# Performance work log

Hardware: AMD Instinct MI355X
Metric: run time of the kernel (lower is better)

The kernel has to match this reference:

```python
import jax, jax.numpy as jnp
import numpy as np

B, S, V, H, NH, DFF, L, T = 16, 256, 30522, 768, 12, 3072, 12, 9
DH = H // NH
LN_EPS = 1e-12


def _ln(x, g, b):
    m = x.mean(-1, keepdims=True)
    v = ((x - m) ** 2).mean(-1, keepdims=True)
    return (x - m) * jax.lax.rsqrt(v + LN_EPS) * g + b


def setup_inputs() -> dict:
    key = jax.random.key(0)
    ks = jax.random.split(key, 20)
    n = lambda k, shp: jax.random.normal(k, shp, jnp.float32) * 0.02
    return {
        "x": jax.random.randint(ks[0], (B, S), 0, V),
        "target": jax.random.randint(ks[1], (B, S), 0, T),
        "word_emb": n(ks[2], (V, H)),
        "pos_emb": n(ks[3], (S, H)),
        "type_emb": n(ks[4], (2, H)),
        "emb_ln_g": jnp.ones((H,)), "emb_ln_b": jnp.zeros((H,)),
        "Wq": n(ks[5], (L, H, H)), "bq": jnp.zeros((L, H)),
        "Wk": n(ks[6], (L, H, H)), "bk": jnp.zeros((L, H)),
        "Wv": n(ks[7], (L, H, H)), "bv": jnp.zeros((L, H)),
        "Wo": n(ks[8], (L, H, H)), "bo": jnp.zeros((L, H)),
        "ln1_g": jnp.ones((L, H)), "ln1_b": jnp.zeros((L, H)),
        "W1": n(ks[9], (L, H, DFF)), "b1": jnp.zeros((L, DFF)),
        "W2": n(ks[10], (L, DFF, H)), "b2": jnp.zeros((L, H)),
        "ln2_g": jnp.ones((L, H)), "ln2_b": jnp.zeros((L, H)),
        "clf_W": n(ks[11], (H, T)), "clf_b": jnp.zeros((T,)),
        "crf_start": jax.random.uniform(ks[12], (T,), jnp.float32, -0.1, 0.1),
        "crf_trans": jax.random.uniform(ks[13], (T, T), jnp.float32, -0.1, 0.1),
        "crf_end": jax.random.uniform(ks[14], (T,), jnp.float32, -0.1, 0.1),
    }


def _forward(x, target, word_emb, pos_emb, type_emb, emb_ln_g, emb_ln_b,
             Wq, bq, Wk, bk, Wv, bv, Wo, bo, ln1_g, ln1_b,
             W1, b1, W2, b2, ln2_g, ln2_b, clf_W, clf_b,
             crf_start, crf_trans, crf_end):
    # ---- BERT-base encoder (post-LN), no attention mask (all tokens valid) ----
    h = _ln(word_emb[x] + pos_emb[None, :, :] + type_emb[0][None, None, :], emb_ln_g, emb_ln_b)
    scale = 1.0 / np.sqrt(DH).astype(np.float32)
    for l in range(L):
        q = (h @ Wq[l] + bq[l]).reshape(B, S, NH, DH)
        k = (h @ Wk[l] + bk[l]).reshape(B, S, NH, DH)
        v = (h @ Wv[l] + bv[l]).reshape(B, S, NH, DH)
        att = jax.nn.softmax(jnp.einsum('bqhd,bkhd->bhqk', q, k) * scale, axis=-1)
        ctx = jnp.einsum('bhqk,bkhd->bqhd', att, v).reshape(B, S, H)
        h = _ln(h + ctx @ Wo[l] + bo[l], ln1_g[l], ln1_b[l])
        ff = jax.nn.gelu(h @ W1[l] + b1[l], approximate=False) @ W2[l] + b2[l]
        h = _ln(h + ff, ln2_g[l], ln2_b[l])

    logits = h @ clf_W + clf_b  # [B,S,T] emissions

    # ---- CRF negative log-likelihood (torchcrf semantics, reduction='mean') ----
    mask = target > -1                      # [B,S] bool
    tags = jnp.where(mask, target, 0)
    bidx = jnp.arange(B)
    emit = jnp.take_along_axis(logits, tags[..., None], axis=-1)[..., 0]  # [B,S]

    # numerator: score of the gold path
    num = crf_start[tags[:, 0]] + emit[:, 0]
    trans = crf_trans[tags[:, :-1], tags[:, 1:]]                          # [B,S-1]
    num = num + jnp.sum((trans + emit[:, 1:]) * mask[:, 1:], axis=1)
    last = jnp.sum(mask.astype(jnp.int32), axis=1) - 1
    num = num + crf_end[tags[bidx, last]]

    # denominator: forward algorithm (logsumexp recurrence over time)
    alpha0 = crf_start[None, :] + logits[:, 0]                            # [B,T]

    def step(alpha, xs):
        em, m = xs                                                        # [B,T], [B]
        nxt = jax.nn.logsumexp(alpha[:, :, None] + crf_trans[None], axis=1) + em
        return jnp.where(m[:, None], nxt, alpha), None

    alpha, _ = jax.lax.scan(step, alpha0,
                            (jnp.swapaxes(logits[:, 1:], 0, 1),
                             jnp.swapaxes(mask[:, 1:], 0, 1)))
    denom = jax.nn.logsumexp(alpha + crf_end[None, :], axis=1)

    llh = num - denom
    return -jnp.mean(llh)  # model returns -loss where loss = mean log-likelihood


def reference(x, target, word_emb, pos_emb, type_emb, emb_ln_g, emb_ln_b,
              Wq, bq, Wk, bk, Wv, bv, Wo, bo, ln1_g, ln1_b,
              W1, b1, W2, b2, ln2_g, ln2_b, clf_W, clf_b,
              crf_start, crf_trans, crf_end):
    return _forward(x, target, word_emb, pos_emb, type_emb, emb_ln_g, emb_ln_b,
                    Wq, bq, Wk, bk, Wv, bv, Wo, bo, ln1_g, ln1_b,
                    W1, b1, W2, b2, ln2_g, ln2_b, clf_W, clf_b,
                    crf_start, crf_trans, crf_end)
```

## Files before the change

### kernel.cpp

```cpp
#include <hip/hip_runtime.h>
#include <math.h>

#define B 16
#define S 256
#define H 768
#define NH 12
#define DH 64
#define DFF 3072
#define L 12
#define T 9
#define M (B*S)
#define LN_EPS 1e-12f
#define QKVS (3*H)
#define NCH 16

typedef __attribute__((ext_vector_type(8))) __bf16 bf16x8;
typedef __attribute__((ext_vector_type(8))) unsigned short u16x8;
typedef __attribute__((ext_vector_type(4))) unsigned short u16x4;
typedef __attribute__((ext_vector_type(4))) float f32x4;

__device__ __forceinline__ unsigned short f2bf(float f) {
    unsigned int u = __float_as_uint(f);
    unsigned int r = u + 0x7fffu + ((u >> 16) & 1u);
    return (unsigned short)(r >> 16);
}
__device__ __forceinline__ float bf2f(unsigned short h) {
    return __uint_as_float((unsigned int)h << 16);
}

__global__ void convT_kernel(const float* __restrict__ W, unsigned short* __restrict__ WT,
                             int K, int N, size_t dstLayerStride) {
    __shared__ float tile[32][33];
    const int layer = blockIdx.z;
    const float* Wp = W + (size_t)layer * K * N;
    unsigned short* Tp = WT + (size_t)layer * dstLayerStride;
    const int n0 = blockIdx.x * 32, k0 = blockIdx.y * 32;
    const int tx = threadIdx.x, ty = threadIdx.y;
#pragma unroll
    for (int i = 0; i < 32; i += 8)
        tile[ty + i][tx] = Wp[(size_t)(k0 + ty + i) * N + n0 + tx];
    __syncthreads();
    {
        const int u = ty * 32 + tx;
        const int r = u >> 3, kq = (u & 7) << 2;
        u16x4 o;
#pragma unroll
        for (int j = 0; j < 4; ++j) o[j] = f2bf(tile[kq + j][r]);
        *(u16x4*)&Tp[(size_t)(n0 + r) * K + k0 + kq] = o;
    }
}

__global__ void biascat_kernel(const float* __restrict__ bq, const float* __restrict__ bk,
                               const float* __restrict__ bv, float* __restrict__ out) {
    int idx = blockIdx.x * 256 + threadIdx.x;
    if (idx >= L * QKVS) return;
    int l = idx / QKVS, c = idx % QKVS;
    float v = (c < H) ? bq[l * H + c] : (c < 2 * H) ? bk[l * H + c - H] : bv[l * H + c - 2 * H];
    out[idx] = v;
}

__global__ void embed_ln_kernel(const int* __restrict__ x,
                                const float* __restrict__ word_emb,
                                const float* __restrict__ pos_emb,
                                const float* __restrict__ type_emb,
                                const float* __restrict__ g,
                                const float* __restrict__ bta,
                                float* __restrict__ h,
                                unsigned short* __restrict__ hb) {
    const int row = blockIdx.x;
    const int s = row % S;
    const int tok = x[row];
    const int t = threadIdx.x;
    const int c = t << 2;
    const float4 wv = *(const float4*)&word_emb[(size_t)tok * H + c];
    const float4 pv = *(const float4*)&pos_emb[s * H + c];
    const float4 tv = *(const float4*)&type_emb[c];
    float v[4] = {wv.x + pv.x + tv.x, wv.y + pv.y + tv.y, wv.z + pv.z + tv.z, wv.w + pv.w + tv.w};
    float s1 = v[0] + v[1] + v[2] + v[3];
    float s2 = v[0]*v[0] + v[1]*v[1] + v[2]*v[2] + v[3]*v[3];
#pragma unroll
    for (int o = 32; o; o >>= 1) { s1 += __shfl_xor(s1, o); s2 += __shfl_xor(s2, o); }
    __shared__ float ws[3][2];
    const int w = t >> 6, l = t & 63;
    if (l == 0) { ws[w][0] = s1; ws[w][1] = s2; }
    __syncthreads();
    const float S1 = ws[0][0] + ws[1][0] + ws[2][0];
    const float S2 = ws[0][1] + ws[1][1] + ws[2][1];
    const float mean = S1 * (1.0f / H);
    const float var = fmaxf(S2 * (1.0f / H) - mean * mean, 0.f);
    const float inv = rsqrtf(var + LN_EPS);
    const float4 gv = *(const float4*)&g[c];
    const float4 bv = *(const float4*)&bta[c];
    float4 outv;
    outv.x = (v[0] - mean) * inv * gv.x + bv.x;
    outv.y = (v[1] - mean) * inv * gv.y + bv.y;
    outv.z = (v[2] - mean) * inv * gv.z + bv.z;
    outv.w = (v[3] - mean) * inv * gv.w + bv.w;
    *(float4*)&h[(size_t)row * H + c] = outv;
    u16x4 ob = {f2bf(outv.x), f2bf(outv.y), f2bf(outv.z), f2bf(outv.w)};
    *(u16x4*)&hb[(size_t)row * H + c] = ob;
}

__global__ void residual_ln_kernel(float* __restrict__ h,
                                   const unsigned short* __restrict__ delta,
                                   const float* __restrict__ g,
                                   const float* __restrict__ bta,
                                   unsigned short* __restrict__ hb) {
    const int row = blockIdx.x;
    const int t = threadIdx.x;
    const int c = t << 2;
    const float4 hv = *(const float4*)&h[(size_t)row * H + c];
    const u16x4 dv4 = *(const u16x4*)&delta[(size_t)row * H + c];
    float v[4] = {hv.x + bf2f(dv4[0]), hv.y + bf2f(dv4[1]), hv.z + bf2f(dv4[2]), hv.w + bf2f(dv4[3])};
    float s1 = v[0] + v[1] + v[2] + v[3];
    float s2 = v[0]*v[0] + v[1]*v[1] + v[2]*v[2] + v[3]*v[3];
#pragma unroll
    for (int o = 32; o; o >>= 1) { s1 += __shfl_xor(s1, o); s2 += __shfl_xor(s2, o); }
    __shared__ float ws[3][2];
    const int w = t >> 6, l = t & 63;
    if (l == 0) { ws[w][0] = s1; ws[w][1] = s2; }
    __syncthreads();
    const float S1 = ws[0][0] + ws[1][0] + ws[2][0];
    const float S2 = ws[0][1] + ws[1][1] + ws[2][1];
    const float mean = S1 * (1.0f / H);
    const float var = fmaxf(S2 * (1.0f / H) - mean * mean, 0.f);
    const float inv = rsqrtf(var + LN_EPS);
    const float4 gv = *(const float4*)&g[c];
    const float4 bv = *(const float4*)&bta[c];
    float4 outv;
    outv.x = (v[0] - mean) * inv * gv.x + bv.x;
    outv.y = (v[1] - mean) * inv * gv.y + bv.y;
    outv.z = (v[2] - mean) * inv * gv.z + bv.z;
    outv.w = (v[3] - mean) * inv * gv.w + bv.w;
    *(float4*)&h[(size_t)row * H + c] = outv;
    u16x4 ob = {f2bf(outv.x), f2bf(outv.y), f2bf(outv.z), f2bf(outv.w)};
    *(u16x4*)&hb[(size_t)row * H + c] = ob;
}

#define LSTR 72

template<int ACT, int WF, int WB, int MR>
__global__ __launch_bounds__(256, 3)
void gemm_bf16(const unsigned short* __restrict__ A,
               const unsigned short* __restrict__ WT,
               const float* __restrict__ bias,
               float* __restrict__ Cf,
               unsigned short* __restrict__ Cb,
               int K, int N) {
    __shared__ unsigned short lA[MR * 32 * LSTR];
    __shared__ unsigned short lB[128 * LSTR];
    const int tid = threadIdx.x;
    const int m0 = blockIdx.y * (MR * 32), n0 = blockIdx.x << 7;
    const int l = tid & 63, w = tid >> 6;
    const int wr = w >> 1, wc = w & 1;
    const int lr = l & 15, kg = l >> 4;

    const int srow = tid >> 3, scol = (tid & 7) << 3;
    const unsigned short* gA = A + (size_t)(m0 + srow) * K + scol;
    const unsigned short* gB = WT + (size_t)(n0 + srow) * K + scol;

    f32x4 acc[MR][4];
#pragma unroll
    for (int i = 0; i < MR; ++i)
#pragma unroll
        for (int j = 0; j < 4; ++j) acc[i][j] = (f32x4){0.f, 0.f, 0.f, 0.f};

    u16x8 ra[MR], rb[4];
#pragma unroll
    for (int p = 0; p < MR; ++p) ra[p] = *(const u16x8*)(gA + (size_t)p * 32 * K);
#pragma unroll
    for (int p = 0; p < 4; ++p) rb[p] = *(const u16x8*)(gB + (size_t)p * 32 * K);

    for (int kt = 0; kt < K; kt += 64) {
#pragma unroll
        for (int p = 0; p < MR; ++p)
            *(u16x8*)&lA[(srow + p * 32) * LSTR + scol] = ra[p];
#pragma unroll
        for (int p = 0; p < 4; ++p)
            *(u16x8*)&lB[(srow + p * 32) * LSTR + scol] = rb[p];
        __syncthreads();
        if (kt + 64 < K) {
#pragma unroll
            for (int p = 0; p < MR; ++p) ra[p] = *(const u16x8*)(gA + (size_t)p * 32 * K + kt + 64);
#pragma unroll
            for (int p = 0; p < 4; ++p) rb[p] = *(const u16x8*)(gB + (size_t)p * 32 * K + kt + 64);
        }
#pragma unroll
        for (int ks = 0; ks < 2; ++ks) {
            bf16x8 af[MR], bfr[4];
#pragma unroll
            for (int m = 0; m < MR; ++m)
                af[m] = *(const bf16x8*)&lA[(wr * (MR * 16) + (m << 4) + lr) * LSTR + ks * 32 + (kg << 3)];
#pragma unroll
            for (int n = 0; n < 4; ++n)
                bfr[n] = *(const bf16x8*)&lB[((wc << 6) + (n << 4) + lr) * LSTR + ks * 32 + (kg << 3)];
#pragma unroll
            for (int m = 0; m < MR; ++m)
#pragma unroll
                for (int n = 0; n < 4; ++n)
                    acc[m][n] = __builtin_amdgcn_mfma_f32_16x16x32_bf16(af[m], bfr[n], acc[m][n], 0, 0, 0);
        }
        __syncthreads();
    }

    const int rbase = m0 + wr * (MR * 16) + (kg << 2);
    const int cbase = n0 + (wc << 6) + lr;
#pragma unroll
    for (int m = 0; m < MR; ++m) {
#pragma unroll
        for (int n = 0; n < 4; ++n) {
            const int col = cbase + (n << 4);
            const float bv = bias[col];
#pragma unroll
            for (int j = 0; j < 4; ++j) {
                const int row = rbase + (m << 4) + j;
                float v = acc[m][n][j] + bv;
                if (ACT == 1) v = 0.5f * v * (1.0f + erff(v * 0.70710678118654752440f));
                if (WF) Cf[(size_t)row * N + col] = v;
                if (WB) Cb[(size_t)row * N + col] = f2bf(v);
            }
        }
    }
}

__global__ __launch_bounds__(256, 2)
void attn_mfma(const unsigned short* __restrict__ qkv,
               unsigned short* __restrict__ ctxb) {
    __shared__ unsigned short Ks[256 * 72];
    __shared__ unsigned short Vt[64 * 264];
    __shared__ unsigned short Ps[4][16 * 72];

    const int blk = blockIdx.x;
    const int half = blk & 1;
    const int hh = (blk >> 1) % NH;
    const int b = blk / (2 * NH);
    const int t = threadIdx.x;
    const int l = t & 63, w = t >> 6;
    const int l15 = l & 15, g = l >> 4;

    {
        const int c0 = (t & 7) << 3;
        int r = t >> 3;
#pragma unroll
        for (int it = 0; it < 8; ++it, r += 32) {
            u16x8 kv = *(const u16x8*)&qkv[(size_t)(b * S + r) * QKVS + H + hh * 64 + c0];
            *(u16x8*)&Ks[r * 72 + c0] = kv;
        }
    }
    {
        const int d0 = (t & 7) << 3;
        int s = t >> 3;
#pragma unroll
        for (int it = 0; it < 8; ++it, s += 32) {
            u16x8 vv = *(const u16x8*)&qkv[(size_t)(b * S + s) * QKVS + 2 * H + hh * 64 + d0];
#pragma unroll
            for (int j = 0; j < 8; ++j) {
                int d = d0 + j;
                Vt[d * 264 + (s ^ (((d >> 3) & 7) << 3))] = vv[j];
            }
        }
    }
    __syncthreads();

    unsigned short* ps = Ps[w];
#pragma unroll
    for (int qi = 0; qi < 2; ++qi) {
        const int qrow = half * 128 + qi * 64 + w * 16 + l15;
        const unsigned short* qp = &qkv[(size_t)(b * S + qrow) * QKVS + hh * 64 + g * 8];
        bf16x8 aq0 = *(const bf16x8*)qp;
        bf16x8 aq1 = *(const bf16x8*)(qp + 32);

        f32x4 acc[16];
#pragma unroll
        for (int n = 0; n < 16; ++n) acc[n] = (f32x4){0.f, 0.f, 0.f, 0.f};
        __builtin_amdgcn_s_setprio(1);
#pragma unroll
        for (int n = 0; n < 16; ++n) {
            const unsigned short* kp = &Ks[(n * 16 + l15) * 72 + g * 8];
            bf16x8 b0 = *(const bf16x8*)kp;
            bf16x8 b1 = *(const bf16x8*)(kp + 32);
            acc[n] = __builtin_amdgcn_mfma_f32_16x16x32_bf16(aq0, b0, acc[n], 0, 0, 0);
            acc[n] = __builtin_amdgcn_mfma_f32_16x16x32_bf16(aq1, b1, acc[n], 0, 0, 0);
        }
        __builtin_amdgcn_s_setprio(0);

        float inv[4];
#pragma unroll
        for (int j = 0; j < 4; ++j) {
            float mx = acc[0][j];
#pragma unroll
            for (int n = 1; n < 16; ++n) mx = fmaxf(mx, acc[n][j]);
            mx = fmaxf(mx, __shfl_xor(mx, 1));
            mx = fmaxf(mx, __shfl_xor(mx, 2));
            mx = fmaxf(mx, __shfl_xor(mx, 4));
            mx = fmaxf(mx, __shfl_xor(mx, 8));
            float sum = 0.f;
#pragma unroll
            for (int n = 0; n < 16; ++n) {
                float e = exp2f((acc[n][j] - mx) * 0.18033688011112042f);
                acc[n][j] = e;
                sum += e;
            }
            sum += __shfl_xor(sum, 1);
            sum += __shfl_xor(sum, 2);
            sum += __shfl_xor(sum, 4);
            sum += __shfl_xor(sum, 8);
            inv[j] = 1.0f / sum;
        }

        f32x4 cacc[4];
#pragma unroll
        for (int nd = 0; nd < 4; ++nd) cacc[nd] = (f32x4){0.f, 0.f, 0.f, 0.f};
#pragma unroll
        for (int c = 0; c < 4; ++c) {
#pragma unroll
            for (int nl = 0; nl < 4; ++nl) {
                int n = c * 4 + nl;
#pragma unroll
                for (int j = 0; j < 4; ++j)
                    ps[(g * 4 + j) * 72 + nl * 16 + l15] = f2bf(acc[n][j]);
            }
            bf16x8 pa0 = *(const bf16x8*)&ps[l15 * 72 + g * 8];
            bf16x8 pa1 = *(const bf16x8*)&ps[l15 * 72 + 32 + g * 8];
            __builtin_amdgcn_s_setprio(1);
#pragma unroll
            for (int nd = 0; nd < 4; ++nd) {
                const int d = nd * 16 + l15;
                const int swz = ((d >> 3) & 7) << 3;
                const unsigned short* vp0 = &Vt[d * 264 + ((c * 64 + g * 8) ^ swz)];
                const unsigned short* vp1 = &Vt[d * 264 + ((c * 64 + 32 + g * 8) ^ swz)];
                bf16x8 v0 = *(const bf16x8*)vp0;
                bf16x8 v1 = *(const bf16x8*)vp1;
                cacc[nd] = __builtin_amdgcn_mfma_f32_16x16x32_bf16(pa0, v0, cacc[nd], 0, 0, 0);
                cacc[nd] = __builtin_amdgcn_mfma_f32_16x16x32_bf16(pa1, v1, cacc[nd], 0, 0, 0);
            }
            __builtin_amdgcn_s_setprio(0);
        }

#pragma unroll
        for (int nd = 0; nd < 4; ++nd)
#pragma unroll
            for (int j = 0; j < 4; ++j) {
                int qr = half * 128 + qi * 64 + w * 16 + g * 4 + j;
                ctxb[(size_t)(b * S + qr) * H + hh * 64 + nd * 16 + l15] = f2bf(cacc[nd][j] * inv[j]);
            }
    }
}

__global__ void clf_kernel(const float* __restrict__ h,
                           const float* __restrict__ W,
                           const float* __restrict__ bias,
                           float* __restrict__ logits) {
    const int row = blockIdx.x * 4 + (threadIdx.x >> 6);
    const int l = threadIdx.x & 63;
    const float* hp = h + (size_t)row * H;
    float acc[T] = {};
#pragma unroll
    for (int i = 0; i < 12; ++i) {
        const int k = l + (i << 6);
        const float x = hp[k];
        const float* wp = &W[k * T];
#pragma unroll
        for (int n = 0; n < T; ++n) acc[n] += x * wp[n];
    }
#pragma unroll
    for (int o = 32; o; o >>= 1)
#pragma unroll
        for (int n = 0; n < T; ++n) acc[n] += __shfl_xor(acc[n], o);
    if (l < T) logits[(size_t)row * T + l] = acc[l] + bias[l];
}

__global__ void crf_chunk_kernel(const float* __restrict__ logits,
                                 const int* __restrict__ target,
                                 const float* __restrict__ trans,
                                 float* __restrict__ Tc) {
    const int blk = blockIdx.x;
    const int b = blk >> 4, c = blk & 15;
    const int t = threadIdx.x;
    const int i = t / 9, j = t - i * 9;
    const bool act = t < 81;
    __shared__ float Tb[2][81];
    const float* lg = logits + (size_t)b * S * T;
    const int* tg = target + b * S;
    const float K2 = 1.44269504088896340736f;
    const float IK = 0.69314718055994530942f;

    float trc[T];
    if (act) {
#pragma unroll
        for (int k = 0; k < T; ++k) trc[k] = trans[k * T + j];
        Tb[0][t] = (i == j) ? 0.f : -1e30f;
    }
    __syncthreads();

    int p = 0;
    const int s0 = c * 16 + 1;
    const int s1 = (c == 15) ? S : (s0 + 16);
    for (int s = s0; s < s1; ++s) {
        if (tg[s] > -1) {
            if (act) {
                const float em = lg[s * T + j];
                float v[T];
#pragma unroll
                for (int k = 0; k < T; ++k) v[k] = Tb[p][i * 9 + k] + trc[k];
                float mx = fmaxf(v[0], v[1]);
                mx = fmaxf(mx, fmaxf(v[2], v[3]));
                mx = fmaxf(mx, fmaxf(v[4], v[5]));
                mx = fmaxf(mx, fmaxf(v[6], v[7]));
                mx = fmaxf(mx, v[8]);
                float sum = 0.f;
#pragma unroll
                for (int k = 0; k < T; ++k) sum += exp2f((v[k] - mx) * K2);
                Tb[p ^ 1][t] = mx + IK * log2f(sum) + em;
            }
            __syncthreads();
            p ^= 1;
        }
    }
    if (act) Tc[(size_t)blk * 81 + t] = Tb[p][t];
}

__global__ __launch_bounds__(1024)
void crf_final_kernel(const float* __restrict__ logits,
                      const int* __restrict__ target,
                      const float* __restrict__ start,
                      const float* __restrict__ trans,
                      const float* __restrict__ endv,
                      const float* __restrict__ Tc,
                      float* __restrict__ out) {
    const int t = threadIdx.x;
    const int b = t >> 6, l = t & 63;
    const float* lg = logits + (size_t)b * S * T;
    const int* tg = target + b * S;
    const float K2 = 1.44269504088896340736f;
    const float IK = 0.69314718055994530942f;

    float pnum = 0.f; int pcnt = 0;
#pragma unroll
    for (int c = 0; c < 4; ++c) {
        const int s = 1 + l + (c << 6);
        if (s < S) {
            const int tcur = tg[s], tprev = tg[s - 1];
            const bool m = tcur > -1;
            const int tag = m ? tcur : 0;
            const int ptag = (tprev > -1) ? tprev : 0;
            if (m) { pnum += trans[ptag * T + tag] + lg[s * T + tag]; pcnt += 1; }
        }
    }
#pragma unroll
    for (int o = 32; o; o >>= 1) { pnum += __shfl_xor(pnum, o); pcnt += __shfl_xor(pcnt, o); }

    const int jj = (l < T) ? l : 0;
    float a = start[jj] + lg[jj];
    for (int c = 0; c < NCH; ++c) {
        const float* Tm = Tc + ((size_t)(b * NCH + c)) * 81;
        float v[T];
#pragma unroll
        for (int i2 = 0; i2 < T; ++i2) v[i2] = __shfl(a, i2) + Tm[i2 * 9 + jj];
        float mx = fmaxf(v[0], v[1]);
        mx = fmaxf(mx, fmaxf(v[2], v[3]));
        mx = fmaxf(mx, fmaxf(v[4], v[5]));
        mx = fmaxf(mx, fmaxf(v[6], v[7]));
        mx = fmaxf(mx, v[8]);
        float sum = 0.f;
#pragma unroll
        for (int k = 0; k < T; ++k) sum += exp2f((v[k] - mx) * K2);
        a = mx + IK * log2f(sum);
    }

    float val = (l < T) ? (a + endv[jj]) : -1e30f;
    float mx = val;
#pragma unroll
    for (int o = 8; o; o >>= 1) mx = fmaxf(mx, __shfl_xor(mx, o));
    float sm = (l < T) ? exp2f((val - mx) * K2) : 0.f;
#pragma unroll
    for (int o = 8; o; o >>= 1) sm += __shfl_xor(sm, o);
    const float denom = mx + IK * log2f(sm);

    __shared__ float part[16];
    if (l == 0) {
        const bool m0 = tg[0] > -1;
        const int tag0 = m0 ? tg[0] : 0;
        const int cnt = pcnt + (m0 ? 1 : 0);
        int lastIdx = cnt - 1; if (lastIdx < 0) lastIdx = 0;
        const int lt = tg[lastIdx];
        const int lastTag = (lt > -1) ? lt : 0;
        const float num = start[tag0] + lg[tag0] + pnum + endv[lastTag];
        part[b] = num - denom;
    }
    __syncthreads();
    if (t == 0) {
        float s = 0.f;
#pragma unroll
        for (int i = 0; i < 16; ++i) s += part[i];
        out[0] = -s * (1.0f / 16.0f);
    }
}

extern "C" void kernel_launch(void* const* d_in, const int* in_sizes, int n_in,
                              void* d_out, int out_size, void* d_ws, size_t ws_size,
                              hipStream_t stream) {
    const int*   x        = (const int*)d_in[0];
    const int*   target   = (const int*)d_in[1];
    const float* word_emb = (const float*)d_in[2];
    const float* pos_emb  = (const float*)d_in[3];
    const float* type_emb = (const float*)d_in[4];
    const float* emb_ln_g = (const float*)d_in[5];
    const float* emb_ln_b = (const float*)d_in[6];
    const float* Wq = (const float*)d_in[7];
    const float* bq = (const float*)d_in[8];
    const float* Wk = (const float*)d_in[9];
    const float* bk = (const float*)d_in[10];
    const float* Wv = (const float*)d_in[11];
    const float* bv = (const float*)d_in[12];
    const float* Wo = (const float*)d_in[13];
    const float* bo = (const float*)d_in[14];
    const float* ln1_g = (const float*)d_in[15];
    const float* ln1_b = (const float*)d_in[16];
    const float* W1 = (const float*)d_in[17];
    const float* b1 = (const float*)d_in[18];
    const float* W2 = (const float*)d_in[19];
    const float* b2 = (const float*)d_in[20];
    const float* ln2_g = (const float*)d_in[21];
    const float* ln2_b = (const float*)d_in[22];
    const float* clf_W = (const float*)d_in[23];
    const float* clf_b = (const float*)d_in[24];
    const float* crf_start = (const float*)d_in[25];
    const float* crf_trans = (const float*)d_in[26];
    const float* crf_end   = (const float*)d_in[27];

    char* ws = (char*)d_ws;
    size_t off = 0;
    auto alloc = [&](size_t bytes) { void* p = ws + off; off += (bytes + 255) & ~255ull; return p; };

    unsigned short* wqkvT = (unsigned short*)alloc((size_t)L * 3 * H * H * 2);
    unsigned short* woT   = (unsigned short*)alloc((size_t)L * H * H * 2);
    unsigned short* w1T   = (unsigned short*)alloc((size_t)L * H * DFF * 2);
    unsigned short* w2T   = (unsigned short*)alloc((size_t)L * H * DFF * 2);
    float*          bcat  = (float*)alloc((size_t)L * QKVS * 4);
    float*          h     = (float*)alloc((size_t)M * H * 4);
    unsigned short* hb    = (unsigned short*)alloc((size_t)M * H * 2);
    unsigned short* qkvb  = (unsigned short*)alloc((size_t)M * QKVS * 2);
    unsigned short* ctxb  = (unsigned short*)alloc((size_t)M * H * 2);
    unsigned short* gob   = (unsigned short*)alloc((size_t)M * H * 2);
    unsigned short* ffb   = (unsigned short*)alloc((size_t)M * DFF * 2);
    float*          logits = (float*)alloc((size_t)M * T * 4);
    float*          Tcbuf  = (float*)alloc((size_t)B * NCH * 81 * 4);

    dim3 tb(32, 8);
    convT_kernel<<<dim3(H / 32, H / 32, L), tb, 0, stream>>>(Wq, wqkvT,             H, H, (size_t)3 * H * H);
    convT_kernel<<<dim3(H / 32, H / 32, L), tb, 0, stream>>>(Wk, wqkvT + H * H,     H, H, (size_t)3 * H * H);
    convT_kernel<<<dim3(H / 32, H / 32, L), tb, 0, stream>>>(Wv, wqkvT + 2 * H * H, H, H, (size_t)3 * H * H);
    convT_kernel<<<dim3(H / 32, H / 32, L), tb, 0, stream>>>(Wo, woT, H, H, (size_t)H * H);
    convT_kernel<<<dim3(DFF / 32, H / 32, L), tb, 0, stream>>>(W1, w1T, H, DFF, (size_t)H * DFF);
    convT_kernel<<<dim3(H / 32, DFF / 32, L), tb, 0, stream>>>(W2, w2T, DFF, H, (size_t)H * DFF);
    biascat_kernel<<<(L * QKVS + 255) / 256, 256, 0, stream>>>(bq, bk, bv, bcat);

    embed_ln_kernel<<<M, 192, 0, stream>>>(x, word_emb, pos_emb, type_emb, emb_ln_g, emb_ln_b, h, hb);

    const dim3 gQKV(QKVS / 128, M / 128);
    const dim3 gFF1(DFF / 128, M / 128);
    const dim3 gH64(H / 128, M / 64);

    for (int l = 0; l < L; ++l) {
        gemm_bf16<0, 0, 1, 4><<<gQKV, 256, 0, stream>>>(hb, wqkvT + (size_t)l * 3 * H * H, bcat + l * QKVS,
                                                        nullptr, qkvb, H, QKVS);
        attn_mfma<<<B * NH * 2, 256, 0, stream>>>(qkvb, ctxb);
        gemm_bf16<0, 0, 1, 2><<<gH64, 256, 0, stream>>>(ctxb, woT + (size_t)l * H * H, bo + l * H, nullptr, gob, H, H);
        residual_ln_kernel<<<M, 192, 0, stream>>>(h, gob, ln1_g + l * H, ln1_b + l * H, hb);
        gemm_bf16<1, 0, 1, 4><<<gFF1, 256, 0, stream>>>(hb, w1T + (size_t)l * H * DFF, b1 + l * DFF, nullptr, ffb, H, DFF);
        gemm_bf16<0, 0, 1, 2><<<gH64, 256, 0, stream>>>(ffb, w2T + (size_t)l * H * DFF, b2 + l * H, nullptr, gob, DFF, H);
        residual_ln_kernel<<<M, 192, 0, stream>>>(h, gob, ln2_g + l * H, ln2_b + l * H, hb);
    }

    clf_kernel<<<M / 4, 256, 0, stream>>>(h, clf_W, clf_b, logits);
    crf_chunk_kernel<<<B * NCH, 128, 0, stream>>>(logits, target, crf_trans, Tcbuf);
    crf_final_kernel<<<1, 1024, 0, stream>>>(logits, target, crf_start, crf_trans, crf_end, Tcbuf, (float*)d_out);
}
```

Baseline: 1.930 ms.

## Split-K the Wo and FF2 GEMMs and drop the fp32 residual stream

The Wo and FF2 GEMMs, which have few output tiles on the N=768 side, are now split along K into 2 and 4 partitions via blockIdx.z. Each partition writes a bf16 partial sum, and the residual LayerNorm kernel adds the partials together. The fp32 hidden-state copy is removed, so the residual stream, the LN inputs and the classifier all read the bf16 hb buffer. This gives more blocks for occupancy and cuts fp32 traffic. The cost is extra partial-sum writes and reads, plus lost precision from keeping the residual and the partials in bf16.

```diff
diff --git a/kernel.cpp b/kernel.cpp
--- a/kernel.cpp
+++ b/kernel.cpp
@@ -13,6 +13,7 @@
 #define LN_EPS 1e-12f
 #define QKVS (3*H)
 #define NCH 16
+#define MH ((size_t)M * H)
 
 typedef __attribute__((ext_vector_type(8))) __bf16 bf16x8;
 typedef __attribute__((ext_vector_type(8))) unsigned short u16x8;
@@ -65,7 +66,6 @@
                                 const float* __restrict__ type_emb,
                                 const float* __restrict__ g,
                                 const float* __restrict__ bta,
-                                float* __restrict__ h,
                                 unsigned short* __restrict__ hb) {
     const int row = blockIdx.x;
     const int s = row % S;
@@ -91,27 +91,31 @@
     const float inv = rsqrtf(var + LN_EPS);
     const float4 gv = *(const float4*)&g[c];
     const float4 bv = *(const float4*)&bta[c];
-    float4 outv;
-    outv.x = (v[0] - mean) * inv * gv.x + bv.x;
-    outv.y = (v[1] - mean) * inv * gv.y + bv.y;
-    outv.z = (v[2] - mean) * inv * gv.z + bv.z;
-    outv.w = (v[3] - mean) * inv * gv.w + bv.w;
-    *(float4*)&h[(size_t)row * H + c] = outv;
-    u16x4 ob = {f2bf(outv.x), f2bf(outv.y), f2bf(outv.z), f2bf(outv.w)};
+    u16x4 ob;
+    ob[0] = f2bf((v[0] - mean) * inv * gv.x + bv.x);
+    ob[1] = f2bf((v[1] - mean) * inv * gv.y + bv.y);
+    ob[2] = f2bf((v[2] - mean) * inv * gv.z + bv.z);
+    ob[3] = f2bf((v[3] - mean) * inv * gv.w + bv.w);
     *(u16x4*)&hb[(size_t)row * H + c] = ob;
 }
 
-__global__ void residual_ln_kernel(float* __restrict__ h,
+template<int NS>
+__global__ void residual_ln_kernel(unsigned short* __restrict__ hb,
                                    const unsigned short* __restrict__ delta,
                                    const float* __restrict__ g,
-                                   const float* __restrict__ bta,
-                                   unsigned short* __restrict__ hb) {
+                                   const float* __restrict__ bta) {
     const int row = blockIdx.x;
     const int t = threadIdx.x;
     const int c = t << 2;
-    const float4 hv = *(const float4*)&h[(size_t)row * H + c];
-    const u16x4 dv4 = *(const u16x4*)&delta[(size_t)row * H + c];
-    float v[4] = {hv.x + bf2f(dv4[0]), hv.y + bf2f(dv4[1]), hv.z + bf2f(dv4[2]), hv.w + bf2f(dv4[3])};
+    const size_t base = (size_t)row * H + c;
+    const u16x4 hv4 = *(const u16x4*)&hb[base];
+    float v[4] = {bf2f(hv4[0]), bf2f(hv4[1]), bf2f(hv4[2]), bf2f(hv4[3])};
+#pragma unroll
+    for (int sgm = 0; sgm < NS; ++sgm) {
+        const u16x4 dv4 = *(const u16x4*)&delta[sgm * MH + base];
+#pragma unroll
+        for (int j = 0; j < 4; ++j) v[j] += bf2f(dv4[j]);
+    }
     float s1 = v[0] + v[1] + v[2] + v[3];
     float s2 = v[0]*v[0] + v[1]*v[1] + v[2]*v[2] + v[3]*v[3];
 #pragma unroll
@@ -127,37 +131,36 @@
     const float inv = rsqrtf(var + LN_EPS);
     const float4 gv = *(const float4*)&g[c];
     const float4 bv = *(const float4*)&bta[c];
-    float4 outv;
-    outv.x = (v[0] - mean) * inv * gv.x + bv.x;
-    outv.y = (v[1] - mean) * inv * gv.y + bv.y;
-    outv.z = (v[2] - mean) * inv * gv.z + bv.z;
-    outv.w = (v[3] - mean) * inv * gv.w + bv.w;
-    *(float4*)&h[(size_t)row * H + c] = outv;
-    u16x4 ob = {f2bf(outv.x), f2bf(outv.y), f2bf(outv.z), f2bf(outv.w)};
-    *(u16x4*)&hb[(size_t)row * H + c] = ob;
+    u16x4 ob;
+    ob[0] = f2bf((v[0] - mean) * inv * gv.x + bv.x);
+    ob[1] = f2bf((v[1] - mean) * inv * gv.y + bv.y);
+    ob[2] = f2bf((v[2] - mean) * inv * gv.z + bv.z);
+    ob[3] = f2bf((v[3] - mean) * inv * gv.w + bv.w);
+    *(u16x4*)&hb[base] = ob;
 }
 
 #define LSTR 72
 
-template<int ACT, int WF, int WB, int MR>
+template<int ACT, int MR>
 __global__ __launch_bounds__(256, 3)
 void gemm_bf16(const unsigned short* __restrict__ A,
                const unsigned short* __restrict__ WT,
                const float* __restrict__ bias,
-               float* __restrict__ Cf,
                unsigned short* __restrict__ Cb,
-               int K, int N) {
+               int Ksub, int Kfull, int N, size_t splitStride) {
     __shared__ unsigned short lA[MR * 32 * LSTR];
     __shared__ unsigned short lB[128 * LSTR];
     const int tid = threadIdx.x;
+    const int z = blockIdx.z;
     const int m0 = blockIdx.y * (MR * 32), n0 = blockIdx.x << 7;
     const int l = tid & 63, w = tid >> 6;
     const int wr = w >> 1, wc = w & 1;
     const int lr = l & 15, kg = l >> 4;
 
     const int srow = tid >> 3, scol = (tid & 7) << 3;
-    const unsigned short* gA = A + (size_t)(m0 + srow) * K + scol;
-    const unsigned short* gB = WT + (size_t)(n0 + srow) * K + scol;
+    const int kOff = z * Ksub;
+    const unsigned short* gA = A + (size_t)(m0 + srow) * Kfull + kOff + scol;
+    const unsigned short* gB = WT + (size_t)(n0 + srow) * Kfull + kOff + scol;
 
     f32x4 acc[MR][4];
 #pragma unroll
@@ -167,11 +170,11 @@
 
     u16x8 ra[MR], rb[4];
 #pragma unroll
-    for (int p = 0; p < MR; ++p) ra[p] = *(const u16x8*)(gA + (size_t)p * 32 * K);
-#pragma unroll
-    for (int p = 0; p < 4; ++p) rb[p] = *(const u16x8*)(gB + (size_t)p * 32 * K);
-
-    for (int kt = 0; kt < K; kt += 64) {
+    for (int p = 0; p < MR; ++p) ra[p] = *(const u16x8*)(gA + (size_t)p * 32 * Kfull);
+#pragma unroll
+    for (int p = 0; p < 4; ++p) rb[p] = *(const u16x8*)(gB + (size_t)p * 32 * Kfull);
+
+    for (int kt = 0; kt < Ksub; kt += 64) {
 #pragma unroll
         for (int p = 0; p < MR; ++p)
             *(u16x8*)&lA[(srow + p * 32) * LSTR + scol] = ra[p];
@@ -179,11 +182,11 @@
         for (int p = 0; p < 4; ++p)
             *(u16x8*)&lB[(srow + p * 32) * LSTR + scol] = rb[p];
         __syncthreads();
-        if (kt + 64 < K) {
-#pragma unroll
-            for (int p = 0; p < MR; ++p) ra[p] = *(const u16x8*)(gA + (size_t)p * 32 * K + kt + 64);
-#pragma unroll
-            for (int p = 0; p < 4; ++p) rb[p] = *(const u16x8*)(gB + (size_t)p * 32 * K + kt + 64);
+        if (kt + 64 < Ksub) {
+#pragma unroll
+            for (int p = 0; p < MR; ++p) ra[p] = *(const u16x8*)(gA + (size_t)p * 32 * Kfull + kt + 64);
+#pragma unroll
+            for (int p = 0; p < 4; ++p) rb[p] = *(const u16x8*)(gB + (size_t)p * 32 * Kfull + kt + 64);
         }
 #pragma unroll
         for (int ks = 0; ks < 2; ++ks) {
@@ -203,6 +206,7 @@
         __syncthreads();
     }
 
+    unsigned short* Cz = Cb + (size_t)z * splitStride;
     const int rbase = m0 + wr * (MR * 16) + (kg << 2);
     const int cbase = n0 + (wc << 6) + lr;
 #pragma unroll
@@ -210,14 +214,13 @@
 #pragma unroll
         for (int n = 0; n < 4; ++n) {
             const int col = cbase + (n << 4);
-            const float bv = bias[col];
+            const float bv = (z == 0) ? bias[col] : 0.f;
 #pragma unroll
             for (int j = 0; j < 4; ++j) {
                 const int row = rbase + (m << 4) + j;
                 float v = acc[m][n][j] + bv;
                 if (ACT == 1) v = 0.5f * v * (1.0f + erff(v * 0.70710678118654752440f));
-                if (WF) Cf[(size_t)row * N + col] = v;
-                if (WB) Cb[(size_t)row * N + col] = f2bf(v);
+                Cz[(size_t)row * N + col] = f2bf(v);
             }
         }
     }
@@ -347,18 +350,18 @@
     }
 }
 
-__global__ void clf_kernel(const float* __restrict__ h,
+__global__ void clf_kernel(const unsigned short* __restrict__ hb,
                            const float* __restrict__ W,
                            const float* __restrict__ bias,
                            float* __restrict__ logits) {
     const int row = blockIdx.x * 4 + (threadIdx.x >> 6);
     const int l = threadIdx.x & 63;
-    const float* hp = h + (size_t)row * H;
+    const unsigned short* hp = hb + (size_t)row * H;
     float acc[T] = {};
 #pragma unroll
     for (int i = 0; i < 12; ++i) {
         const int k = l + (i << 6);
-        const float x = hp[k];
+        const float x = bf2f(hp[k]);
         const float* wp = &W[k * T];
 #pragma unroll
         for (int n = 0; n < T; ++n) acc[n] += x * wp[n];
@@ -538,11 +541,10 @@
     unsigned short* w1T   = (unsigned short*)alloc((size_t)L * H * DFF * 2);
     unsigned short* w2T   = (unsigned short*)alloc((size_t)L * H * DFF * 2);
     float*          bcat  = (float*)alloc((size_t)L * QKVS * 4);
-    float*          h     = (float*)alloc((size_t)M * H * 4);
-    unsigned short* hb    = (unsigned short*)alloc((size_t)M * H * 2);
+    unsigned short* hb    = (unsigned short*)alloc(MH * 2);
     unsigned short* qkvb  = (unsigned short*)alloc((size_t)M * QKVS * 2);
-    unsigned short* ctxb  = (unsigned short*)alloc((size_t)M * H * 2);
-    unsigned short* gob   = (unsigned short*)alloc((size_t)M * H * 2);
+    unsigned short* ctxb  = (unsigned short*)alloc(MH * 2);
+    unsigned short* gob   = (unsigned short*)alloc(4 * MH * 2);
     unsigned short* ffb   = (unsigned short*)alloc((size_t)M * DFF * 2);
     float*          logits = (float*)alloc((size_t)M * T * 4);
     float*          Tcbuf  = (float*)alloc((size_t)B * NCH * 81 * 4);
@@ -556,24 +558,28 @@
     convT_kernel<<<dim3(H / 32, DFF / 32, L), tb, 0, stream>>>(W2, w2T, DFF, H, (size_t)H * DFF);
     biascat_kernel<<<(L * QKVS + 255) / 256, 256, 0, stream>>>(bq, bk, bv, bcat);
 
-    embed_ln_kernel<<<M, 192, 0, stream>>>(x, word_emb, pos_emb, type_emb, emb_ln_g, emb_ln_b, h, hb);
-
-    const dim3 gQKV(QKVS / 128, M / 128);
-    const dim3 gFF1(DFF / 128, M / 128);
-    const dim3 gH64(H / 128, M / 64);
+    embed_ln_kernel<<<M, 192, 0, stream>>>(x, word_emb, pos_emb, type_emb, emb_ln_g, emb_ln_b, hb);
+
+    const dim3 gQKV(QKVS / 128, M / 128, 1);
+    const dim3 gFF1(DFF / 128, M / 128, 1);
+    const dim3 gWo (H / 128, M / 64, 2);
+    const dim3 gFF2(H / 128, M / 64, 4);
 
     for (int l = 0; l < L; ++l) {
-        gemm_bf16<0, 0, 1, 4><<<gQKV, 256, 0, stream>>>(hb, wqkvT + (size_t)l * 3 * H * H, bcat + l * QKVS,
-                                                        nullptr, qkvb, H, QKVS);
+        gemm_bf16<0, 4><<<gQKV, 256, 0, stream>>>(hb, wqkvT + (size_t)l * 3 * H * H, bcat + l * QKVS,
+                                                  qkvb, H, H, QKVS, 0);
         attn_mfma<<<B * NH * 2, 256, 0, stream>>>(qkvb, ctxb);
-        gemm_bf16<0, 0, 1, 2><<<gH64, 256, 0, stream>>>(ctxb, woT + (size_t)l * H * H, bo + l * H, nullptr, gob, H, H);
-        residual_ln_kernel<<<M, 192, 0, stream>>>(h, gob, ln1_g + l * H, ln1_b + l * H, hb);
-        gemm_bf16<1, 0, 1, 4><<<gFF1, 256, 0, stream>>>(hb, w1T + (size_t)l * H * DFF, b1 + l * DFF, nullptr, ffb, H, DFF);
-        gemm_bf16<0, 0, 1, 2><<<gH64, 256, 0, stream>>>(ffb, w2T + (size_t)l * H * DFF, b2 + l * H, nullptr, gob, DFF, H);
-        residual_ln_kernel<<<M, 192, 0, stream>>>(h, gob, ln2_g + l * H, ln2_b + l * H, hb);
-    }
-
-    clf_kernel<<<M / 4, 256, 0, stream>>>(h, clf_W, clf_b, logits);
+        gemm_bf16<0, 2><<<gWo, 256, 0, stream>>>(ctxb, woT + (size_t)l * H * H, bo + l * H,
+                                                 gob, H / 2, H, H, MH);
+        residual_ln_kernel<2><<<M, 192, 0, stream>>>(hb, gob, ln1_g + l * H, ln1_b + l * H);
+        gemm_bf16<1, 4><<<gFF1, 256, 0, stream>>>(hb, w1T + (size_t)l * H * DFF, b1 + l * DFF,
+                                                  ffb, H, H, DFF, 0);
+        gemm_bf16<0, 2><<<gFF2, 256, 0, stream>>>(ffb, w2T + (size_t)l * H * DFF, b2 + l * H,
+                                                  gob, DFF / 4, DFF, H, MH);
+        residual_ln_kernel<4><<<M, 192, 0, stream>>>(hb, gob, ln2_g + l * H, ln2_b + l * H);
+    }
+
+    clf_kernel<<<M / 4, 256, 0, stream>>>(hb, clf_W, clf_b, logits);
     crf_chunk_kernel<<<B * NCH, 128, 0, stream>>>(logits, target, crf_trans, Tcbuf);
     crf_final_kernel<<<1, 1024, 0, stream>>>(logits, target, crf_start, crf_trans, crf_end, Tcbuf, (float*)d_out);
 }
```

Measured after the change: 1.850 ms. 4.2% less time.
